# Performance work log

Measured on AMD Instinct MI355X. Metric: run time of the kernel, lower is better.

The kernel has to match this reference:

```python
import jax, jax.numpy as jnp
import numpy as np

NUM_HEADS = 16
ROPE_BASE = 10000.0


def _rope(x):
    """Standard rotary embedding. x: (B, H, T, Dh), positions 0..T-1."""
    T, Dh = x.shape[-2], x.shape[-1]
    half = Dh // 2
    inv_freq = 1.0 / (ROPE_BASE ** (jnp.arange(half, dtype=jnp.float32) / half))
    ang = jnp.arange(T, dtype=jnp.float32)[:, None] * inv_freq[None, :]  # (T, half)
    cos, sin = jnp.cos(ang), jnp.sin(ang)
    x1, x2 = x[..., :half], x[..., half:]
    return jnp.concatenate([x1 * cos - x2 * sin, x1 * sin + x2 * cos], axis=-1)


def setup_inputs() -> dict:
    key = jax.random.key(0)
    ks = jax.random.split(key, 5)
    B, N, D = 8, 1025, 1024
    s = 1.0 / np.sqrt(D)
    return {
        "x": jax.random.normal(ks[0], (B, N, D), jnp.float32),
        "wq": jax.random.normal(ks[1], (D, D), jnp.float32) * s,
        "wk": jax.random.normal(ks[2], (D, D), jnp.float32) * s,
        "wv": jax.random.normal(ks[3], (D, D), jnp.float32) * s,
        "q_bias": jnp.zeros((D,), jnp.float32),
        "v_bias": jnp.zeros((D,), jnp.float32),
        "w_out": jax.random.normal(ks[4], (D, D), jnp.float32) * s,
        "b_out": jnp.zeros((D,), jnp.float32),
    }


def reference(x, wq, wk, wv, q_bias, v_bias, w_out, b_out):
    B, N, D = x.shape
    H = NUM_HEADS
    Dh = D // H
    scale = Dh ** -0.5

    q = x @ wq + q_bias           # (B, N, D)
    k = x @ wk
    v = x @ wv + v_bias

    def split_heads(t):  # (B, N, D) -> (B, H, N, Dh)
        return t.reshape(B, N, H, Dh).transpose(0, 2, 1, 3)

    q, k, v = split_heads(q), split_heads(k), split_heads(v)

    # RoPE on all tokens except the first (CLS)
    q = jnp.concatenate([q[:, :, :1, :], _rope(q[:, :, 1:, :])], axis=2)
    k = jnp.concatenate([k[:, :, :1, :], _rope(k[:, :, 1:, :])], axis=2)

    attn = jnp.einsum('bhqd,bhkd->bhqk', q * scale, k)
    attn = jax.nn.softmax(attn, axis=-1)
    out = jnp.einsum('bhqk,bhkd->bhqd', attn, v)  # (B, H, N, Dh)
    out = out.transpose(0, 2, 1, 3).reshape(B, N, D)
    return out @ w_out + b_out
```

## Files before the change

### kernel.cpp

```cpp
#include <hip/hip_runtime.h>

typedef unsigned short u16;
typedef __attribute__((ext_vector_type(8))) short  short8;
typedef __attribute__((ext_vector_type(8))) __bf16 bf16x8;
typedef __attribute__((ext_vector_type(4))) float  f32x4;

#define DEV __device__ __forceinline__

#define BATCH 8
#define SEQ   1025
#define DMODEL 1024
#define NHEAD 16
#define DH    64
#define MROWS (BATCH*SEQ)
#define VPAD  1152
#define KROWS 1088

DEV float bf2f(u16 u) { union { unsigned int i; float f; } v; v.i = ((unsigned int)u) << 16; return v.f; }
DEV u16 f2bf(float f) {
  union { float f; unsigned int i; } v; v.f = f;
  unsigned int x = v.i;
  return (u16)((x + 0x7fffu + ((x >> 16) & 1u)) >> 16);
}

DEV f32x4 mfma16(bf16x8 a, bf16x8 b, f32x4 c) {
  return __builtin_amdgcn_mfma_f32_16x16x32_bf16(a, b, c, 0, 0, 0);
}

DEV void gload_lds16(const void* g, void* s) {
  __builtin_amdgcn_global_load_lds(
      (const __attribute__((address_space(1))) void*)g,
      (__attribute__((address_space(3))) void*)s, 16, 0, 0);
}

DEV float exp2_fast(float x) { float r; asm("v_exp_f32 %0, %1" : "=v"(r) : "v"(x)); return r; }
DEV unsigned cvt_pk_bf16(float lo, float hi) {
  unsigned r;
  asm("v_cvt_pk_bf16_f32 %0, %1, %2" : "=v"(r) : "v"(lo), "v"(hi));
  return r;
}

#define QSCALE (0.125f * 1.44269504088896341f)

__global__ void prep_kernel(const float* __restrict__ x,
                            const float* __restrict__ wq, const float* __restrict__ wk,
                            const float* __restrict__ wv, const float* __restrict__ wo,
                            u16* __restrict__ x_bf, u16* __restrict__ wtqkv,
                            u16* __restrict__ wtout,
                            float* __restrict__ cost, float* __restrict__ sint) {
  __shared__ float tile[64][65];
  const int blk = blockIdx.x, tid = threadIdx.x;
  if (blk < 4100) {
    int i = blk * 256 + tid;
    if (i >= MROWS * 1024 / 8) return;
    const float4* p = (const float4*)x + (size_t)i * 2;
    float4 a = p[0], b = p[1];
    short8 o;
    o[0] = (short)f2bf(a.x); o[1] = (short)f2bf(a.y); o[2] = (short)f2bf(a.z); o[3] = (short)f2bf(a.w);
    o[4] = (short)f2bf(b.x); o[5] = (short)f2bf(b.y); o[6] = (short)f2bf(b.z); o[7] = (short)f2bf(b.w);
    *(short8*)(x_bf + (size_t)i * 8) = o;
  } else if (blk < 5124) {
    int wg = blk - 4100;
    int z = wg >> 8, rem = wg & 255;
    int kx = rem & 15, ny = rem >> 4;
    const float* src = (z == 0) ? wq : (z == 1) ? wk : (z == 2) ? wv : wo;
    int k0 = kx * 64, n0 = ny * 64;
    int c = tid & 63, rq = tid >> 6;
#pragma unroll
    for (int p = 0; p < 16; ++p) {
      int r = p * 4 + rq;
      tile[r][c] = src[(size_t)(k0 + r) * 1024 + n0 + c];
    }
    __syncthreads();
    u16* dst = (z < 3) ? (wtqkv + (size_t)z * 1024 * 1024) : wtout;
#pragma unroll
    for (int p = 0; p < 16; ++p) {
      int r = p * 4 + rq;
      dst[(size_t)(n0 + r) * 1024 + k0 + c] = f2bf(tile[c][r]);
    }
  } else {
    int i = (blk - 5124) * 256 + tid;
    if (i >= 1024 * 32) return;
    int pos = i >> 5, d = i & 31;
    float inv = powf(10000.0f, -(float)d / 32.0f);
    float ang = (float)pos * inv;
    cost[i] = cosf(ang);
    sint[i] = sinf(ang);
  }
}

DEV void stage_issue(const u16* __restrict__ gtile, char* dst, int wid, int lane, int s) {
  int tt = wid * 64 + lane;
  int row = s * 64 + (tt >> 3);
  int cs = (((tt & 7) ^ (row & 7)) << 3);
  gload_lds16(gtile + (size_t)row * 1024 + cs, dst + s * 8192 + wid * 1024);
}

__global__ __launch_bounds__(512, 2) void gemm256(const u16* __restrict__ A,
    const u16* __restrict__ Bw, u16* __restrict__ Cout) {
  __shared__ char lds[131072];
  int mt, nt;
  {
    int orig = blockIdx.x;
    int xcd = orig & 7;
    int f = (xcd < 4 ? xcd * 50 : 200 + (xcd - 4) * 49) + (orig >> 3);
    if (f < 384) { int sr = f / 48, rem = f % 48; nt = rem >> 2; mt = sr * 4 + (rem & 3); }
    else { mt = 32; nt = f - 384; }
  }
  const int t = threadIdx.x;
  const int wid = t >> 6, lane = t & 63;
  const int l4 = lane >> 4, l15 = lane & 15;
  const int wrow = wid >> 2, wcol = wid & 3;
  const long rowA0 = (long)mt * 256;
  const long rowB0 = (long)nt * 256;

  f32x4 acc[8][4];
#pragma unroll
  for (int m = 0; m < 8; ++m)
#pragma unroll
    for (int n = 0; n < 4; ++n) { f32x4 z = {0.f,0.f,0.f,0.f}; acc[m][n] = z; }

#pragma unroll
  for (int s = 0; s < 4; ++s) stage_issue(A  + rowA0 * 1024, lds,         wid, lane, s);
#pragma unroll
  for (int s = 0; s < 4; ++s) stage_issue(Bw + rowB0 * 1024, lds + 65536, wid, lane, s);
  asm volatile("s_waitcnt vmcnt(0)" ::: "memory");
  __syncthreads();

  int cur = 0;
  for (int kt = 0; kt < 16; ++kt) {
    const char* Al = lds + cur * 32768;
    const char* Bl = lds + 65536 + cur * 32768;
    char* An = lds + (cur ^ 1) * 32768;
    char* Bn = lds + 65536 + (cur ^ 1) * 32768;
    const u16* gA = A  + rowA0 * 1024 + (kt + 1) * 64;
    const u16* gB = Bw + rowB0 * 1024 + (kt + 1) * 64;
    const bool pf = kt < 15;

#pragma unroll
    for (int kk = 0; kk < 2; ++kk) {
      bf16x8 bfr[4];
#pragma unroll
      for (int n = 0; n < 4; ++n) {
        int r = wcol * 64 + n * 16 + l15;
        bfr[n] = *(const bf16x8*)(Bl + r * 128 + ((kk * 64 + l4 * 16) ^ ((r & 7) << 4)));
      }
#pragma unroll
      for (int mh = 0; mh < 2; ++mh) {
        if (pf) {
          if (kk == 0 && mh == 0) { stage_issue(gA, An, wid, lane, 0); stage_issue(gA, An, wid, lane, 1); }
          if (kk == 0 && mh == 1) { stage_issue(gA, An, wid, lane, 2); stage_issue(gA, An, wid, lane, 3); }
          if (kk == 1 && mh == 0) { stage_issue(gB, Bn, wid, lane, 0); stage_issue(gB, Bn, wid, lane, 1); }
          if (kk == 1 && mh == 1) { stage_issue(gB, Bn, wid, lane, 2); stage_issue(gB, Bn, wid, lane, 3); }
        }
        bf16x8 af[4];
#pragma unroll
        for (int m = 0; m < 4; ++m) {
          int r = wrow * 128 + (mh * 4 + m) * 16 + l15;
          af[m] = *(const bf16x8*)(Al + r * 128 + ((kk * 64 + l4 * 16) ^ ((r & 7) << 4)));
        }
        __builtin_amdgcn_s_setprio(1);
#pragma unroll
        for (int m = 0; m < 4; ++m)
#pragma unroll
          for (int n = 0; n < 4; ++n)
            acc[mh * 4 + m][n] = mfma16(af[m], bfr[n], acc[mh * 4 + m][n]);
        __builtin_amdgcn_s_setprio(0);
      }
    }
    asm volatile("s_waitcnt vmcnt(0)" ::: "memory");
    __syncthreads();
    cur ^= 1;
  }

#pragma unroll
  for (int m = 0; m < 8; ++m)
#pragma unroll
    for (int rg = 0; rg < 4; ++rg) {
      long row = rowA0 + wrow * 128 + m * 16 + l4 * 4 + rg;
      if (row >= MROWS) continue;
#pragma unroll
      for (int n = 0; n < 4; ++n) {
        long col = rowB0 + wcol * 64 + n * 16 + l15;
        Cout[row * 3072 + col] = f2bf(acc[m][n][rg]);
      }
    }
}

DEV void map_tiles(int f, int MT, int NT, int& mt, int& nt) {
  int body = (MT & ~7) * NT;
  if (f >= body) { int r = f - body; mt = (MT & ~7) + r / NT; nt = r % NT; }
  else { int sr = f / (8 * NT); int rem = f - sr * 8 * NT; nt = rem >> 3; mt = sr * 8 + (rem & 7); }
}

__global__ __launch_bounds__(256) void gemm_out(const u16* __restrict__ A,
    const u16* __restrict__ Bw, float* __restrict__ Cout, const float* __restrict__ bias) {
  __shared__ char smem[32768];
  int mt, nt;
  { int wg = blockIdx.x; int f = (wg & 7) * 65 + (wg >> 3); map_tiles(f, 65, 8, mt, nt); }
  const int t = threadIdx.x;
  const int wid = t >> 6, lane = t & 63;
  const int l4 = lane >> 4, l15 = lane & 15;
  const int wr = wid >> 1, wc = wid & 1;
  const long rowA0 = (long)mt * 128;
  const long rowB0 = (long)nt * 128;

  f32x4 acc[4][4];
#pragma unroll
  for (int m = 0; m < 4; ++m)
#pragma unroll
    for (int n = 0; n < 4; ++n) { f32x4 z = {0.f,0.f,0.f,0.f}; acc[m][n] = z; }

  const int srow = t >> 3;
  const int scol = (t & 7) * 8;

  for (int k0 = 0; k0 < 1024; k0 += 64) {
    __syncthreads();
#pragma unroll
    for (int i = 0; i < 4; ++i) {
      const u16* ga = A  + (rowA0 + i * 32 + srow) * 1024 + k0 + scol;
      gload_lds16(ga, smem + i * 4096 + wid * 1024);
      const u16* gb = Bw + (rowB0 + i * 32 + srow) * 1024 + k0 + scol;
      gload_lds16(gb, smem + 16384 + i * 4096 + wid * 1024);
    }
    __syncthreads();

    bf16x8 af[4][2], bfr[4][2];
#pragma unroll
    for (int m = 0; m < 4; ++m)
#pragma unroll
      for (int kk = 0; kk < 2; ++kk)
        af[m][kk] = *(const bf16x8*)(smem + (wr * 64 + m * 16 + l15) * 128 + kk * 64 + l4 * 16);
#pragma unroll
    for (int n = 0; n < 4; ++n)
#pragma unroll
      for (int kk = 0; kk < 2; ++kk)
        bfr[n][kk] = *(const bf16x8*)(smem + 16384 + (wc * 64 + n * 16 + l15) * 128 + kk * 64 + l4 * 16);

#pragma unroll
    for (int m = 0; m < 4; ++m)
#pragma unroll
      for (int n = 0; n < 4; ++n)
#pragma unroll
        for (int kk = 0; kk < 2; ++kk)
          acc[m][n] = mfma16(af[m][kk], bfr[n][kk], acc[m][n]);
  }

#pragma unroll
  for (int m = 0; m < 4; ++m)
#pragma unroll
    for (int rg = 0; rg < 4; ++rg) {
      long row = rowA0 + wr * 64 + m * 16 + l4 * 4 + rg;
      if (row >= MROWS) continue;
#pragma unroll
      for (int n = 0; n < 4; ++n) {
        long col = rowB0 + wc * 64 + n * 16 + l15;
        Cout[row * 1024 + col] = acc[m][n][rg] + bias[col];
      }
    }
}

__global__ void postqkv_kernel(const u16* __restrict__ cq, const float* __restrict__ qb,
                               const float* __restrict__ vb,
                               const float* __restrict__ cost, const float* __restrict__ sint,
                               u16* __restrict__ Qh, u16* __restrict__ Kh,
                               u16* __restrict__ VTh) {
  __shared__ float tile[64][65];
  const int blk = blockIdx.x, tid = threadIdx.x;
  if (blk < 513) {
    int idx = blk * 256 + tid;
    if (idx >= MROWS * NHEAD) return;
    int h = idx & 15, row = idx >> 4;
    int b = row / SEQ, n = row - b * SEQ;
    const u16* src = cq + (size_t)row * 3072 + h * 64;
    size_t dq = ((size_t)(b * 16 + h) * SEQ   + n) * 64;
    size_t dk = ((size_t)(b * 16 + h) * KROWS + n) * 64;
    bool dorope = (n > 0);
    const float* ct = cost + (size_t)(n - 1) * 32;
    const float* st = sint + (size_t)(n - 1) * 32;
#pragma unroll
    for (int i = 0; i < 4; ++i) {
      short8 qlo = *(const short8*)(src + i * 8);
      short8 qhi = *(const short8*)(src + 32 + i * 8);
      short8 klo = *(const short8*)(src + 1024 + i * 8);
      short8 khi = *(const short8*)(src + 1024 + 32 + i * 8);
      short8 oqlo, oqhi, oklo, okhi;
#pragma unroll
      for (int j = 0; j < 8; ++j) {
        int d = i * 8 + j;
        float q1 = bf2f((u16)qlo[j]) + qb[h * 64 + d];
        float q2 = bf2f((u16)qhi[j]) + qb[h * 64 + 32 + d];
        float k1 = bf2f((u16)klo[j]);
        float k2 = bf2f((u16)khi[j]);
        float c = dorope ? ct[d] : 1.0f;
        float s = dorope ? st[d] : 0.0f;
        oqlo[j] = (short)f2bf((q1 * c - q2 * s) * QSCALE);
        oqhi[j] = (short)f2bf((q1 * s + q2 * c) * QSCALE);
        oklo[j] = (short)f2bf(k1 * c - k2 * s);
        okhi[j] = (short)f2bf(k1 * s + k2 * c);
      }
      *(short8*)(Qh + dq + i * 8)      = oqlo;
      *(short8*)(Qh + dq + 32 + i * 8) = oqhi;
      *(short8*)(Kh + dk + i * 8)      = oklo;
      *(short8*)(Kh + dk + 32 + i * 8) = okhi;
    }
  } else {
    int wg = blk - 513;
    int bh = wg / 18, nx = wg - bh * 18;
    int b = bh >> 4, h = bh & 15;
    int n0 = nx * 64;
    int c = tid & 63, rq = tid >> 6;
#pragma unroll
    for (int p = 0; p < 16; ++p) {
      int r = p * 4 + rq;
      int n = n0 + r;
      float v = 0.f;
      if (n < SEQ) v = bf2f(cq[(size_t)(b * SEQ + n) * 3072 + 2048 + h * 64 + c]) + vb[h * 64 + c];
      tile[r][c] = v;
    }
    __syncthreads();
#pragma unroll
    for (int p = 0; p < 16; ++p) {
      int d = p * 4 + rq;
      VTh[((size_t)bh * 64 + d) * VPAD + n0 + c] = f2bf(tile[c][d]);
    }
  }
}

DEV void stage_rows(const u16* __restrict__ g, size_t strideElems, char* lbase,
                    int wid, int lane) {
#pragma unroll
  for (int s = 0; s < 2; ++s) {
    int off = s * 4096 + wid * 1024 + lane * 16;
    int r = off >> 7, cs = (off >> 4) & 7;
    const u16* src = g + (size_t)r * strideElems + ((cs ^ (r & 7)) << 3);
    gload_lds16(src, lbase + s * 4096 + wid * 1024);
  }
}

__global__ __launch_bounds__(256, 4) void attn128(const u16* __restrict__ Qh,
    const u16* __restrict__ Kh, const u16* __restrict__ VTh,
    u16* __restrict__ xattn) {
  __shared__ char lds[32768];
  const int wg = blockIdx.x;
  const int x = (wg & 7) * 144 + (wg >> 3);
  const int qt = x % 9, bh = x / 9;
  const int b = bh >> 4, h = bh & 15;
  const int t = threadIdx.x, w = t >> 6, lane = t & 63;
  const int l4 = lane >> 4, l15 = lane & 15;
  const u16* Qb = Qh + (size_t)bh * (SEQ * 64);
  const u16* Kb = Kh + (size_t)bh * (KROWS * 64);
  const u16* Vb = VTh + (size_t)bh * (64 * VPAD);
  const int q0 = qt * 128 + w * 32;
  const int srcb = l15 + ((l4 & 1) << 5);
  const bool hi4 = (l4 >> 1) != 0;

  bf16x8 aq[2][2];
#pragma unroll
  for (int m = 0; m < 2; ++m) {
    int qr = q0 + m * 16 + l15; if (qr > SEQ - 1) qr = SEQ - 1;
    aq[m][0] = *(const bf16x8*)(Qb + (size_t)qr * 64 + l4 * 8);
    aq[m][1] = *(const bf16x8*)(Qb + (size_t)qr * 64 + 32 + l4 * 8);
  }
  bf16x8 ones;
  { union { unsigned u[4]; bf16x8 v; } ou;
    ou.u[0] = ou.u[1] = ou.u[2] = ou.u[3] = 0x3F803F80u; ones = ou.v; }

  f32x4 o[2][4], osum[2];
  float mrow[2];
#pragma unroll
  for (int m = 0; m < 2; ++m) {
#pragma unroll
    for (int n = 0; n < 4; ++n) { f32x4 z = {0.f,0.f,0.f,0.f}; o[m][n] = z; }
    f32x4 z = {0.f,0.f,0.f,0.f}; osum[m] = z;
    mrow[m] = -1e30f;
  }

  stage_rows(Kb, 64, lds, w, lane);
  stage_rows(Vb, VPAD, lds + 16384, w, lane);
  asm volatile("s_waitcnt vmcnt(0)" ::: "memory");
  __syncthreads();

  int cur = 0;
  for (int kt = 0; kt < 17; ++kt) {
    const int kb = kt * 64;
    if (kt < 16) {
      stage_rows(Kb + (size_t)(kb + 64) * 64, 64, lds + (cur ^ 1) * 8192, w, lane);
      stage_rows(Vb + (kb + 64), VPAD, lds + 16384 + (cur ^ 1) * 8192, w, lane);
    }
    const char* Kl = lds + cur * 8192;
    const char* Vl = lds + 16384 + cur * 8192;

    f32x4 s[2][4];
#pragma unroll
    for (int tt = 0; tt < 4; ++tt) {
      const int kr = tt * 16 + l15;
      const char* kp = Kl + kr * 128;
      bf16x8 bk0 = *(const bf16x8*)(kp + ((l4       ^ (kr & 7)) << 4));
      bf16x8 bk1 = *(const bf16x8*)(kp + (((4 + l4) ^ (kr & 7)) << 4));
#pragma unroll
      for (int m = 0; m < 2; ++m) {
        f32x4 z = {0.f,0.f,0.f,0.f};
        z = mfma16(bk0, aq[m][0], z);
        z = mfma16(bk1, aq[m][1], z);
        s[m][tt] = z;
      }
    }

    if (kt == 16) {
#pragma unroll
      for (int m = 0; m < 2; ++m) {
        s[m][0][0] = (l4 == 0) ? s[m][0][0] : -1e30f;
        s[m][0][1] = -1e30f; s[m][0][2] = -1e30f; s[m][0][3] = -1e30f;
#pragma unroll
        for (int tt = 1; tt < 4; ++tt) {
          s[m][tt][0] = -1e30f; s[m][tt][1] = -1e30f; s[m][tt][2] = -1e30f; s[m][tt][3] = -1e30f;
        }
      }
    }

    float tmax[2];
#pragma unroll
    for (int m = 0; m < 2; ++m) {
      float a0 = fmaxf(fmaxf(s[m][0][0], s[m][0][1]), fmaxf(s[m][0][2], s[m][0][3]));
      float a1 = fmaxf(fmaxf(s[m][1][0], s[m][1][1]), fmaxf(s[m][1][2], s[m][1][3]));
      float a2 = fmaxf(fmaxf(s[m][2][0], s[m][2][1]), fmaxf(s[m][2][2], s[m][2][3]));
      float a3 = fmaxf(fmaxf(s[m][3][0], s[m][3][1]), fmaxf(s[m][3][2], s[m][3][3]));
      float tm = fmaxf(fmaxf(a0, a1), fmaxf(a2, a3));
      tm = fmaxf(tm, __shfl_xor(tm, 16));
      tm = fmaxf(tm, __shfl_xor(tm, 32));
      tmax[m] = tm;
    }

    int needR = (tmax[0] > mrow[0] + 8.0f) || (tmax[1] > mrow[1] + 8.0f);
    if (__any(needR)) {
#pragma unroll
      for (int m = 0; m < 2; ++m) {
        float mnew = fmaxf(mrow[m], tmax[m]);
        float alpha = exp2_fast(mrow[m] - mnew);
        mrow[m] = mnew;
        float al[4];
#pragma unroll
        for (int rg = 0; rg < 4; ++rg) al[rg] = __shfl(alpha, l4 * 4 + rg);
#pragma unroll
        for (int n = 0; n < 4; ++n)
#pragma unroll
          for (int rg = 0; rg < 4; ++rg) o[m][n][rg] *= al[rg];
#pragma unroll
        for (int rg = 0; rg < 4; ++rg) osum[m][rg] *= al[rg];
      }
    }

    unsigned pk[2][4][2];
#pragma unroll
    for (int m = 0; m < 2; ++m)
#pragma unroll
      for (int tt = 0; tt < 4; ++tt) {
        float p0 = exp2_fast(s[m][tt][0] - mrow[m]);
        float p1 = exp2_fast(s[m][tt][1] - mrow[m]);
        float p2 = exp2_fast(s[m][tt][2] - mrow[m]);
        float p3 = exp2_fast(s[m][tt][3] - mrow[m]);
        pk[m][tt][0] = cvt_pk_bf16(p0, p1);
        pk[m][tt][1] = cvt_pk_bf16(p2, p3);
      }

#pragma unroll
    for (int kk = 0; kk < 2; ++kk) {
      bf16x8 pa[2];
#pragma unroll
      for (int m = 0; m < 2; ++m) {
        union { unsigned u[4]; bf16x8 v; } pu;
#pragma unroll
        for (int bb = 0; bb < 2; ++bb)
#pragma unroll
          for (int pr = 0; pr < 2; ++pr) {
            unsigned t0 = (unsigned)__shfl((int)pk[m][2 * kk][pr],     srcb + bb * 16);
            unsigned t1 = (unsigned)__shfl((int)pk[m][2 * kk + 1][pr], srcb + bb * 16);
            pu.u[bb * 2 + pr] = hi4 ? t1 : t0;
          }
        pa[m] = pu.v;
      }
#pragma unroll
      for (int n = 0; n < 4; ++n) {
        const int vr = n * 16 + l15;
        bf16x8 bv = *(const bf16x8*)(Vl + vr * 128 + (((kk * 4 + l4) ^ (vr & 7)) << 4));
#pragma unroll
        for (int m = 0; m < 2; ++m)
          o[m][n] = mfma16(pa[m], bv, o[m][n]);
      }
#pragma unroll
      for (int m = 0; m < 2; ++m)
        osum[m] = mfma16(pa[m], ones, osum[m]);
    }

    asm volatile("s_waitcnt vmcnt(0)" ::: "memory");
    __syncthreads();
    cur ^= 1;
  }

#pragma unroll
  for (int m = 0; m < 2; ++m)
#pragma unroll
    for (int n = 0; n < 4; ++n)
#pragma unroll
      for (int rg = 0; rg < 4; ++rg) {
        int qrow = q0 + m * 16 + l4 * 4 + rg;
        if (qrow < SEQ)
          xattn[(size_t)(b * SEQ + qrow) * 1024 + h * 64 + n * 16 + l15] =
              f2bf(o[m][n][rg] / osum[m][rg]);
      }
}


extern "C" void kernel_launch(void* const* d_in, const int* in_sizes, int n_in,
                              void* d_out, int out_size, void* d_ws, size_t ws_size,
                              hipStream_t stream) {
  const float* x      = (const float*)d_in[0];
  const float* wq     = (const float*)d_in[1];
  const float* wk     = (const float*)d_in[2];
  const float* wv     = (const float*)d_in[3];
  const float* q_bias = (const float*)d_in[4];
  const float* v_bias = (const float*)d_in[5];
  const float* w_out  = (const float*)d_in[6];
  const float* b_out  = (const float*)d_in[7];

  char* ws = (char*)d_ws;
  size_t off = 0;
  auto alc = [&](size_t bytes) { size_t r = off; off += (bytes + 255) & ~(size_t)255; return r; };

  u16*  x_bf  = (u16*)(ws + alc((size_t)MROWS * 1024 * 2));
  u16*  wtqkv = (u16*)(ws + alc((size_t)3072 * 1024 * 2));
  u16*  wtout = (u16*)(ws + alc((size_t)1024 * 1024 * 2));
  u16*  xattn = (u16*)(ws + alc((size_t)MROWS * 1024 * 2));
  u16*  cqkv  = (u16*)(ws + alc((size_t)8448 * 3072 * 2));
  u16*  Qhp   = (u16*)(ws + alc((size_t)128 * SEQ * 64 * 2));
  u16*  Khp   = (u16*)(ws + alc((size_t)128 * KROWS * 64 * 2));
  u16*  VThp  = (u16*)(ws + alc((size_t)128 * 64 * VPAD * 2));
  float* cost = (float*)(ws + alc((size_t)1024 * 32 * 4));
  float* sint = (float*)(ws + alc((size_t)1024 * 32 * 4));
  (void)ws_size; (void)in_sizes; (void)n_in; (void)out_size;

  prep_kernel<<<dim3(5252), 256, 0, stream>>>(x, wq, wk, wv, w_out,
                                              x_bf, wtqkv, wtout, cost, sint);
  gemm256<<<dim3(396), 512, 0, stream>>>(x_bf, wtqkv, cqkv);
  postqkv_kernel<<<dim3(513 + 2304), 256, 0, stream>>>(cqkv, q_bias, v_bias,
                                                       cost, sint, Qhp, Khp, VThp);
  attn128<<<dim3(1152), 256, 0, stream>>>(Qhp, Khp, VThp, xattn);
  gemm_out<<<dim3(520), 256, 0, stream>>>(xattn, wtout, (float*)d_out, b_out);
}
```

Measured before the change: 249.1 us.

## Restructure QKV GEMM mainloop into fine-grained half-panel pipeline with partial waitcnt fences

Replaces the double-buffered 64-wide K loop, which waited on all loads (vmcnt(0)) plus a full barrier once per K step, with a schedule that stages 32-wide half panels of A and B. Each half panel is followed by a partial vmcnt fence and barrier, so global-to-LDS loads stay in flight across several MFMA quads instead of draining each iteration. The LDS layout changes to 64-byte rows with a new XOR swizzle. The cost is more barriers per K step and hand-counted vmcnt values that must match the number of outstanding loads exactly.

```diff
diff --git a/kernel.cpp b/kernel.cpp
--- a/kernel.cpp
+++ b/kernel.cpp
@@ -89,16 +89,47 @@
   }
 }
 
-DEV void stage_issue(const u16* __restrict__ gtile, char* dst, int wid, int lane, int s) {
-  int tt = wid * 64 + lane;
-  int row = s * 64 + (tt >> 3);
-  int cs = (((tt & 7) ^ (row & 7)) << 3);
-  gload_lds16(gtile + (size_t)row * 1024 + cs, dst + s * 8192 + wid * 1024);
+#define FENCE(N) asm volatile("s_waitcnt vmcnt(" N ") lgkmcnt(0)\n\ts_barrier" ::: "memory")
+
+DEV void stage_half(const u16* __restrict__ gpanel, long row0, int kcol,
+                    char* dst, int wid, int lane) {
+#pragma unroll
+  for (int s = 0; s < 2; ++s) {
+    int tt = wid * 64 + lane;
+    int row = s * 128 + (tt >> 2), c2 = tt & 3;
+    const u16* src = gpanel + (row0 + row) * 1024 + kcol + ((c2 ^ ((row >> 1) & 3)) << 3);
+    gload_lds16(src, dst + s * 8192 + wid * 1024);
+  }
+}
+
+DEV void quad(const char* sm, int buf, int kk, int mh, int wrow, int wcol,
+              int l4, int l15, f32x4 (&acc)[8][4]) {
+  const char* Ab = sm + buf * 65536 + kk * 16384;
+  const char* Bb = sm + buf * 65536 + 32768 + kk * 16384;
+  bf16x8 bfr[4];
+#pragma unroll
+  for (int n = 0; n < 4; ++n) {
+    int r = wcol * 64 + n * 16 + l15;
+    bfr[n] = *(const bf16x8*)(Bb + r * 64 + ((l4 << 4) ^ (((r >> 1) & 3) << 4)));
+  }
+  bf16x8 af[4];
+#pragma unroll
+  for (int m = 0; m < 4; ++m) {
+    int r = wrow * 128 + (mh * 4 + m) * 16 + l15;
+    af[m] = *(const bf16x8*)(Ab + r * 64 + ((l4 << 4) ^ (((r >> 1) & 3) << 4)));
+  }
+  __builtin_amdgcn_s_setprio(1);
+#pragma unroll
+  for (int m = 0; m < 4; ++m)
+#pragma unroll
+    for (int n = 0; n < 4; ++n)
+      acc[mh * 4 + m][n] = mfma16(af[m], bfr[n], acc[mh * 4 + m][n]);
+  __builtin_amdgcn_s_setprio(0);
 }
 
 __global__ __launch_bounds__(512, 2) void gemm256(const u16* __restrict__ A,
     const u16* __restrict__ Bw, u16* __restrict__ Cout) {
-  __shared__ char lds[131072];
+  __shared__ char smem[131072];
   int mt, nt;
   {
     int orig = blockIdx.x;
@@ -120,57 +151,32 @@
 #pragma unroll
     for (int n = 0; n < 4; ++n) { f32x4 z = {0.f,0.f,0.f,0.f}; acc[m][n] = z; }
 
-#pragma unroll
-  for (int s = 0; s < 4; ++s) stage_issue(A  + rowA0 * 1024, lds,         wid, lane, s);
-#pragma unroll
-  for (int s = 0; s < 4; ++s) stage_issue(Bw + rowB0 * 1024, lds + 65536, wid, lane, s);
-  asm volatile("s_waitcnt vmcnt(0)" ::: "memory");
-  __syncthreads();
-
-  int cur = 0;
-  for (int kt = 0; kt < 16; ++kt) {
-    const char* Al = lds + cur * 32768;
-    const char* Bl = lds + 65536 + cur * 32768;
-    char* An = lds + (cur ^ 1) * 32768;
-    char* Bn = lds + 65536 + (cur ^ 1) * 32768;
-    const u16* gA = A  + rowA0 * 1024 + (kt + 1) * 64;
-    const u16* gB = Bw + rowB0 * 1024 + (kt + 1) * 64;
-    const bool pf = kt < 15;
-
-#pragma unroll
-    for (int kk = 0; kk < 2; ++kk) {
-      bf16x8 bfr[4];
-#pragma unroll
-      for (int n = 0; n < 4; ++n) {
-        int r = wcol * 64 + n * 16 + l15;
-        bfr[n] = *(const bf16x8*)(Bl + r * 128 + ((kk * 64 + l4 * 16) ^ ((r & 7) << 4)));
-      }
-#pragma unroll
-      for (int mh = 0; mh < 2; ++mh) {
-        if (pf) {
-          if (kk == 0 && mh == 0) { stage_issue(gA, An, wid, lane, 0); stage_issue(gA, An, wid, lane, 1); }
-          if (kk == 0 && mh == 1) { stage_issue(gA, An, wid, lane, 2); stage_issue(gA, An, wid, lane, 3); }
-          if (kk == 1 && mh == 0) { stage_issue(gB, Bn, wid, lane, 0); stage_issue(gB, Bn, wid, lane, 1); }
-          if (kk == 1 && mh == 1) { stage_issue(gB, Bn, wid, lane, 2); stage_issue(gB, Bn, wid, lane, 3); }
-        }
-        bf16x8 af[4];
-#pragma unroll
-        for (int m = 0; m < 4; ++m) {
-          int r = wrow * 128 + (mh * 4 + m) * 16 + l15;
-          af[m] = *(const bf16x8*)(Al + r * 128 + ((kk * 64 + l4 * 16) ^ ((r & 7) << 4)));
-        }
-        __builtin_amdgcn_s_setprio(1);
-#pragma unroll
-        for (int m = 0; m < 4; ++m)
-#pragma unroll
-          for (int n = 0; n < 4; ++n)
-            acc[mh * 4 + m][n] = mfma16(af[m], bfr[n], acc[mh * 4 + m][n]);
-        __builtin_amdgcn_s_setprio(0);
-      }
-    }
-    asm volatile("s_waitcnt vmcnt(0)" ::: "memory");
-    __syncthreads();
-    cur ^= 1;
+  stage_half(A,  rowA0, 0,  smem + 0,     wid, lane);
+  stage_half(Bw, rowB0, 0,  smem + 32768, wid, lane);
+  stage_half(A,  rowA0, 32, smem + 16384, wid, lane);
+  stage_half(Bw, rowB0, 32, smem + 49152, wid, lane);
+
+  for (int j = 0; j < 7; ++j) {
+    const int cY = (2 * j + 1) * 64, cX = (2 * j + 2) * 64;
+    FENCE("4"); stage_half(A,  rowA0, cY,      smem + 65536 + 0,     wid, lane); quad(smem, 0, 0, 0, wrow, wcol, l4, l15, acc);
+    FENCE("6"); stage_half(Bw, rowB0, cY,      smem + 65536 + 32768, wid, lane); quad(smem, 0, 0, 1, wrow, wcol, l4, l15, acc);
+    FENCE("4"); stage_half(A,  rowA0, cY + 32, smem + 65536 + 16384, wid, lane); quad(smem, 0, 1, 0, wrow, wcol, l4, l15, acc);
+    FENCE("6"); stage_half(Bw, rowB0, cY + 32, smem + 65536 + 49152, wid, lane); quad(smem, 0, 1, 1, wrow, wcol, l4, l15, acc);
+    FENCE("4"); stage_half(A,  rowA0, cX,      smem + 0,     wid, lane); quad(smem, 1, 0, 0, wrow, wcol, l4, l15, acc);
+    FENCE("6"); stage_half(Bw, rowB0, cX,      smem + 32768, wid, lane); quad(smem, 1, 0, 1, wrow, wcol, l4, l15, acc);
+    FENCE("4"); stage_half(A,  rowA0, cX + 32, smem + 16384, wid, lane); quad(smem, 1, 1, 0, wrow, wcol, l4, l15, acc);
+    FENCE("6"); stage_half(Bw, rowB0, cX + 32, smem + 49152, wid, lane); quad(smem, 1, 1, 1, wrow, wcol, l4, l15, acc);
+  }
+  {
+    const int cY = 15 * 64;
+    FENCE("4"); stage_half(A,  rowA0, cY,      smem + 65536 + 0,     wid, lane); quad(smem, 0, 0, 0, wrow, wcol, l4, l15, acc);
+    FENCE("6"); stage_half(Bw, rowB0, cY,      smem + 65536 + 32768, wid, lane); quad(smem, 0, 0, 1, wrow, wcol, l4, l15, acc);
+    FENCE("4"); stage_half(A,  rowA0, cY + 32, smem + 65536 + 16384, wid, lane); quad(smem, 0, 1, 0, wrow, wcol, l4, l15, acc);
+    FENCE("6"); stage_half(Bw, rowB0, cY + 32, smem + 65536 + 49152, wid, lane); quad(smem, 0, 1, 1, wrow, wcol, l4, l15, acc);
+    FENCE("4"); quad(smem, 1, 0, 0, wrow, wcol, l4, l15, acc);
+    FENCE("4"); quad(smem, 1, 0, 1, wrow, wcol, l4, l15, acc);
+    FENCE("0"); quad(smem, 1, 1, 0, wrow, wcol, l4, l15, acc);
+    FENCE("0"); quad(smem, 1, 1, 1, wrow, wcol, l4, l15, acc);
   }
 
 #pragma unroll
```

After: 247.3 us. Within noise of the previous version (-0.7%).
